# Kernel optimization log

Measured on AMD Instinct MI355X. Metric: run time of the kernel, lower is better.

Reference implementation:

```python
import jax, jax.numpy as jnp
import numpy as np

NUM_HEADS = 8


def _conv1(x, w, b):
    # 1x1x1 Conv3d == per-voxel channel linear map. x: [B,C,D,H,W], w: [O,C], b: [O]
    return jnp.einsum('bcdhw,oc->bodhw', x, w) + b[None, :, None, None, None]


def setup_inputs() -> dict:
    key = jax.random.key(0)
    ks = jax.random.split(key, 7)
    B, C, D, H, W = 1, 64, 16, 16, 16
    s = 0.02
    return {
        'decoder_features': jax.random.normal(ks[0], (B, C, D, H, W), jnp.float32),
        'mae_features': jax.random.normal(ks[1], (B, C, D, H, W), jnp.float32),
        'q_w': jax.random.normal(ks[2], (C, C), jnp.float32) * s,
        'q_b': jnp.zeros((C,), jnp.float32),
        'k_w': jax.random.normal(ks[3], (C, C), jnp.float32) * s,
        'k_b': jnp.zeros((C,), jnp.float32),
        'v_w': jax.random.normal(ks[4], (C, C), jnp.float32) * s,
        'v_b': jnp.zeros((C,), jnp.float32),
        'o_w': jax.random.normal(ks[5], (C, C), jnp.float32) * s,
        'o_b': jnp.zeros((C,), jnp.float32),
    }


def reference(decoder_features, mae_features, q_w, q_b, k_w, k_b, v_w, v_b, o_w, o_b):
    B, C, D, H, W = decoder_features.shape
    nh = NUM_HEADS
    hd = C // nh
    N = D * H * W
    scale = hd ** -0.5

    def split_heads(x):
        # [B,C,D,H,W] -> [B, nh, N, hd]
        return x.reshape(B, nh, hd, N).transpose(0, 1, 3, 2)

    Q = split_heads(_conv1(decoder_features, q_w, q_b))
    K = split_heads(_conv1(mae_features, k_w, k_b))
    V = split_heads(_conv1(mae_features, v_w, v_b))

    attn = jax.nn.softmax(jnp.einsum('bhnc,bhmc->bhnm', Q, K) * scale, axis=-1)
    out = jnp.einsum('bhnm,bhmc->bhnc', attn, V)  # [B, nh, N, hd]
    out = out.transpose(0, 1, 3, 2).reshape(B, C, D, H, W)
    return _conv1(out, o_w, o_b)
```

## Files before the change

kernel.cpp:

```cpp
#include <hip/hip_runtime.h>
#include <hip/hip_bf16.h>
#include <math.h>


#define N_VOX 4096
#define NH 8
#define QSCALE 0.51010813f

typedef unsigned short ushort_t;
typedef __attribute__((ext_vector_type(8))) short bf16x8;
typedef __attribute__((ext_vector_type(16))) float f32x16;

__device__ __forceinline__ unsigned short f2bf(float f) {
  union { float f; unsigned u; } v; v.f = f;
  unsigned r = v.u + 0x7FFFu + ((v.u >> 16) & 1u);
  return (unsigned short)(r >> 16);
}
__device__ __forceinline__ unsigned pk2bf(float a, float b) {
  __hip_bfloat162 h = __float22bfloat162_rn(float2{a, b});
  union { __hip_bfloat162 h; unsigned u; } c; c.h = h;
  return c.u;
}
__device__ __forceinline__ float ex2(float x) { return __builtin_amdgcn_exp2f(x); }

__global__ __launch_bounds__(256) void qkv_pack(
    const float* __restrict__ dec, const float* __restrict__ mae,
    const float* __restrict__ qw, const float* __restrict__ qb_,
    const float* __restrict__ kw, const float* __restrict__ kb,
    const float* __restrict__ vw, const float* __restrict__ vb,
    ushort_t* __restrict__ Qp, ushort_t* __restrict__ Kp,
    ushort_t* __restrict__ VtP, ushort_t* __restrict__ zeroblk) {
  const int bx = blockIdx.x;
  const int n = blockIdx.y * 256 + threadIdx.x;

  if (bx < 8) {
    const int h = bx;
    float x[64];
#pragma unroll
    for (int c = 0; c < 64; ++c) x[c] = dec[c * N_VOX + n];
    float qv[8];
#pragma unroll
    for (int j = 0; j < 8; ++j) {
      const int o = h * 8 + j;
      float a = qb_[o];
#pragma unroll
      for (int c = 0; c < 64; ++c) a = fmaf(x[c], qw[o * 64 + c], a);
      qv[j] = a * QSCALE;
    }
    uint4 pk;
    pk.x = pk2bf(qv[0], qv[1]); pk.y = pk2bf(qv[2], qv[3]);
    pk.z = pk2bf(qv[4], qv[5]); pk.w = pk2bf(qv[6], qv[7]);
    *(uint4*)(Qp + ((size_t)h * N_VOX + n) * 8) = pk;
  } else {
    const int h = bx - 8;
    float x[64];
#pragma unroll
    for (int c = 0; c < 64; ++c) x[c] = mae[c * N_VOX + n];
    float kv[8], vv[8];
#pragma unroll
    for (int j = 0; j < 8; ++j) {
      const int o = h * 8 + j;
      float a = kb[o], b = vb[o];
#pragma unroll
      for (int c = 0; c < 64; ++c) {
        a = fmaf(x[c], kw[o * 64 + c], a);
        b = fmaf(x[c], vw[o * 64 + c], b);
      }
      kv[j] = a; vv[j] = b;
    }
    uint4 pk;
    pk.x = pk2bf(kv[0], kv[1]); pk.y = pk2bf(kv[2], kv[3]);
    pk.z = pk2bf(kv[4], kv[5]); pk.w = pk2bf(kv[6], kv[7]);
    *(uint4*)(Kp + ((size_t)h * N_VOX + n) * 8) = pk;

    const size_t base =
        (((size_t)h * (N_VOX / 16) + (n >> 4)) * 64 + ((n >> 3) & 1) * 32) * 8 +
        (n & 7);
#pragma unroll
    for (int d = 0; d < 8; ++d) VtP[base + (size_t)d * 8] = f2bf(vv[d]);
    VtP[base + 8 * 8] = 0x3F80;
    if (h == 0 && n < 8) zeroblk[n] = 0;
  }
}

__global__ __launch_bounds__(256, 4) void attn_mfma(
    const ushort_t* __restrict__ Qp, const ushort_t* __restrict__ Kp,
    const ushort_t* __restrict__ VtP, const ushort_t* __restrict__ zeroblk,
    float* __restrict__ o_part, int kps) {
  const int tid = threadIdx.x;
  const int lane = tid & 63;
  const int wave = tid >> 6;
  const int l31 = lane & 31;
  const int lhalf = lane >> 5;
  const int h = blockIdx.y;
  const int ks = blockIdx.z;
  const int qb = blockIdx.x * 256 + wave * 64;

  __shared__ ushort_t P_lds[8][32 * 36];

  bf16x8 qfrag0 = *(const bf16x8*)(Qp + ((size_t)h * N_VOX + qb + l31) * 8);
  bf16x8 qfrag1 = *(const bf16x8*)(Qp + ((size_t)h * N_VOX + qb + 32 + l31) * 8);

  f32x16 zf, acc0, acc1;
#pragma unroll
  for (int i = 0; i < 16; ++i) { zf[i] = 0.f; acc0[i] = 0.f; acc1[i] = 0.f; }

  const ushort_t* KpH = Kp + (size_t)h * N_VOX * 8;
  const ushort_t* VtPH = VtP + (size_t)h * (N_VOX / 16) * 64 * 8;
  ushort_t* pb0 = &P_lds[wave * 2 + 0][l31 * 36];
  ushort_t* pb1 = &P_lds[wave * 2 + 1][l31 * 36];

  const int kbeg = ks * kps;
  const ushort_t* kzero = zeroblk;

  bf16x8 kf = *(const bf16x8*)(lhalf ? kzero
                                     : (KpH + (size_t)(kbeg + l31) * 8));
  bf16x8 vf0 = *(const bf16x8*)(VtPH + ((size_t)((kbeg >> 4) + 0) * 64 + lane) * 8);
  bf16x8 vf1 = *(const bf16x8*)(VtPH + ((size_t)((kbeg >> 4) + 1) * 64 + lane) * 8);

  for (int kk = 0; kk < kps; kk += 32) {
    const int knext = (kk + 32 < kps) ? (kbeg + kk + 32) : (kbeg + kk);
    bf16x8 kf_n = *(const bf16x8*)(lhalf ? kzero
                                         : (KpH + (size_t)(knext + l31) * 8));
    bf16x8 vf0_n = *(const bf16x8*)(VtPH + ((size_t)((knext >> 4) + 0) * 64 + lane) * 8);
    bf16x8 vf1_n = *(const bf16x8*)(VtPH + ((size_t)((knext >> 4) + 1) * 64 + lane) * 8);

    f32x16 s0 = __builtin_amdgcn_mfma_f32_32x32x16_bf16(kf, qfrag0, zf, 0, 0, 0);
    f32x16 s1 = __builtin_amdgcn_mfma_f32_32x32x16_bf16(kf, qfrag1, zf, 0, 0, 0);

#pragma unroll
    for (int G = 0; G < 4; ++G) {
      uint2 w;
      w.x = pk2bf(ex2(s0[G * 4 + 0]), ex2(s0[G * 4 + 1]));
      w.y = pk2bf(ex2(s0[G * 4 + 2]), ex2(s0[G * 4 + 3]));
      *(uint2*)(pb0 + G * 8 + lhalf * 4) = w;
    }
#pragma unroll
    for (int G = 0; G < 4; ++G) {
      uint2 w;
      w.x = pk2bf(ex2(s1[G * 4 + 0]), ex2(s1[G * 4 + 1]));
      w.y = pk2bf(ex2(s1[G * 4 + 2]), ex2(s1[G * 4 + 3]));
      *(uint2*)(pb1 + G * 8 + lhalf * 4) = w;
    }

#pragma unroll
    for (int grp = 0; grp < 2; ++grp) {
      union { bf16x8 v; uint2 u[2]; } p0, p1;
      p0.u[0] = *(const uint2*)(pb0 + grp * 16 + lhalf * 8);
      p0.u[1] = *(const uint2*)(pb0 + grp * 16 + lhalf * 8 + 4);
      p1.u[0] = *(const uint2*)(pb1 + grp * 16 + lhalf * 8);
      p1.u[1] = *(const uint2*)(pb1 + grp * 16 + lhalf * 8 + 4);
      const bf16x8 vf = grp ? vf1 : vf0;
      acc0 = __builtin_amdgcn_mfma_f32_32x32x16_bf16(p0.v, vf, acc0, 0, 0, 0);
      acc1 = __builtin_amdgcn_mfma_f32_32x32x16_bf16(p1.v, vf, acc1, 0, 0, 0);
    }

    kf = kf_n; vf0 = vf0_n; vf1 = vf1_n;
  }

  if (l31 < 9) {
    float* ob = o_part + ((size_t)(ks * NH + h) * 9 + l31) * N_VOX;
#pragma unroll
    for (int t = 0; t < 2; ++t) {
      const f32x16 a = t ? acc1 : acc0;
      const int qst = qb + t * 32 + 4 * lhalf;
#pragma unroll
      for (int G = 0; G < 4; ++G) {
        float4 v4 = make_float4(a[G * 4 + 0], a[G * 4 + 1], a[G * 4 + 2], a[G * 4 + 3]);
        *(float4*)(ob + qst + 8 * G) = v4;
      }
    }
  }
}

__global__ __launch_bounds__(256) void combine(
    const float* __restrict__ o_part, float* __restrict__ ocomb, int KS) {
  const int t = blockIdx.x * 256 + threadIdx.x;
  const int c = t >> 12, n = t & (N_VOX - 1);
  const int h = c >> 3, d = c & 7;
  float so = 0.f, sl = 0.f;
  for (int s = 0; s < KS; ++s) {
    const float* base = o_part + ((size_t)(s * NH + h) * 9) * N_VOX;
    so += base[d * N_VOX + n];
    sl += base[8 * N_VOX + n];
  }
  ocomb[(size_t)c * N_VOX + n] = so / sl;
}

__global__ __launch_bounds__(256) void out_proj(
    const float* __restrict__ ocomb, const float* __restrict__ ow,
    const float* __restrict__ obias, float* __restrict__ out) {
  const int og = blockIdx.x;
  const int n = blockIdx.y * 256 + threadIdx.x;
  float x[64];
#pragma unroll
  for (int c = 0; c < 64; ++c) x[c] = ocomb[c * N_VOX + n];
#pragma unroll
  for (int j = 0; j < 8; ++j) {
    const int o = og * 8 + j;
    float acc = obias[o];
#pragma unroll
    for (int c = 0; c < 64; ++c) acc = fmaf(x[c], ow[o * 64 + c], acc);
    out[o * N_VOX + n] = acc;
  }
}

extern "C" void kernel_launch(void* const* d_in, const int* in_sizes, int n_in,
                              void* d_out, int out_size, void* d_ws, size_t ws_size,
                              hipStream_t stream) {
  const float* dec = (const float*)d_in[0];
  const float* mae = (const float*)d_in[1];
  const float* qw = (const float*)d_in[2];
  const float* qb = (const float*)d_in[3];
  const float* kw = (const float*)d_in[4];
  const float* kb = (const float*)d_in[5];
  const float* vw = (const float*)d_in[6];
  const float* vb = (const float*)d_in[7];
  const float* ow = (const float*)d_in[8];
  const float* ob = (const float*)d_in[9];
  float* out = (float*)d_out;
  char* ws = (char*)d_ws;

  const size_t OFF_QP = 0;
  const size_t OFF_KP = 0x80000;
  const size_t OFF_ZERO = 0x100000;
  const size_t OFF_VT = 0x101000;
  const size_t OFF_OPART = 0x301000;

  int KS = 16;
  while (KS > 1) {
    size_t need = OFF_OPART + (size_t)KS * NH * 9 * N_VOX * 4 + 64ull * N_VOX * 4;
    if (need <= ws_size) break;
    KS >>= 1;
  }
  const size_t OFF_OCOMB = OFF_OPART + (size_t)KS * NH * 9 * N_VOX * 4;

  ushort_t* Qp = (ushort_t*)(ws + OFF_QP);
  ushort_t* Kp = (ushort_t*)(ws + OFF_KP);
  ushort_t* zb = (ushort_t*)(ws + OFF_ZERO);
  ushort_t* VtP = (ushort_t*)(ws + OFF_VT);
  float* o_part = (float*)(ws + OFF_OPART);
  float* ocomb = (float*)(ws + OFF_OCOMB);

  qkv_pack<<<dim3(16, 16), 256, 0, stream>>>(dec, mae, qw, qb, kw, kb, vw, vb,
                                             Qp, Kp, VtP, zb);
  attn_mfma<<<dim3(16, 8, KS), 256, 0, stream>>>(Qp, Kp, VtP, zb, o_part,
                                                 N_VOX / KS);
  combine<<<1024, 256, 0, stream>>>(o_part, ocomb, KS);
  out_proj<<<dim3(8, 16), 256, 0, stream>>>(ocomb, ow, ob, out);
}
```

Baseline: 137.0 us.

## Fuse combine into output projection, fix split count, zero-pad K rows

Merges the split-K combine and the output 1x1 projection into one kernel that sums partial outputs and normalises them on the fly, removing the intermediate buffer and one launch. The split count is fixed at compile time to 8 (previously up to 16, depending on workspace size). K rows are padded to 16 elements with zeros so the upper half-wave loads zeros directly instead of branching to a shared zero block. The software prefetch of K/V in the attention loop is dropped in favour of plain per-iteration loads. The fused kernel rereads o_part once for each of the 8 output groups, and the lost prefetch may expose load latency.

```diff
diff --git a/kernel.cpp b/kernel.cpp
--- a/kernel.cpp
+++ b/kernel.cpp
@@ -5,6 +5,8 @@
 
 #define N_VOX 4096
 #define NH 8
+#define KS 8
+#define KPS (N_VOX / KS)
 #define QSCALE 0.51010813f
 
 typedef unsigned short ushort_t;
@@ -28,8 +30,8 @@
     const float* __restrict__ qw, const float* __restrict__ qb_,
     const float* __restrict__ kw, const float* __restrict__ kb,
     const float* __restrict__ vw, const float* __restrict__ vb,
-    ushort_t* __restrict__ Qp, ushort_t* __restrict__ Kp,
-    ushort_t* __restrict__ VtP, ushort_t* __restrict__ zeroblk) {
+    ushort_t* __restrict__ Qp, ushort_t* __restrict__ KpZ,
+    ushort_t* __restrict__ VtP) {
   const int bx = blockIdx.x;
   const int n = blockIdx.y * 256 + threadIdx.x;
 
@@ -60,18 +62,20 @@
 #pragma unroll
     for (int j = 0; j < 8; ++j) {
       const int o = h * 8 + j;
-      float a = kb[o], b = vb[o];
+      float a = kb[o], v = vb[o];
 #pragma unroll
       for (int c = 0; c < 64; ++c) {
         a = fmaf(x[c], kw[o * 64 + c], a);
-        b = fmaf(x[c], vw[o * 64 + c], b);
+        v = fmaf(x[c], vw[o * 64 + c], v);
       }
-      kv[j] = a; vv[j] = b;
+      kv[j] = a; vv[j] = v;
     }
     uint4 pk;
     pk.x = pk2bf(kv[0], kv[1]); pk.y = pk2bf(kv[2], kv[3]);
     pk.z = pk2bf(kv[4], kv[5]); pk.w = pk2bf(kv[6], kv[7]);
-    *(uint4*)(Kp + ((size_t)h * N_VOX + n) * 8) = pk;
+    ushort_t* krow = KpZ + ((size_t)h * N_VOX + n) * 16;
+    *(uint4*)(krow) = pk;
+    *(uint4*)(krow + 8) = make_uint4(0, 0, 0, 0);
 
     const size_t base =
         (((size_t)h * (N_VOX / 16) + (n >> 4)) * 64 + ((n >> 3) & 1) * 32) * 8 +
@@ -79,14 +83,12 @@
 #pragma unroll
     for (int d = 0; d < 8; ++d) VtP[base + (size_t)d * 8] = f2bf(vv[d]);
     VtP[base + 8 * 8] = 0x3F80;
-    if (h == 0 && n < 8) zeroblk[n] = 0;
   }
 }
 
 __global__ __launch_bounds__(256, 4) void attn_mfma(
-    const ushort_t* __restrict__ Qp, const ushort_t* __restrict__ Kp,
-    const ushort_t* __restrict__ VtP, const ushort_t* __restrict__ zeroblk,
-    float* __restrict__ o_part, int kps) {
+    const ushort_t* __restrict__ Qp, const ushort_t* __restrict__ KpZ,
+    const ushort_t* __restrict__ VtP, float* __restrict__ o_part) {
   const int tid = threadIdx.x;
   const int lane = tid & 63;
   const int wave = tid >> 6;
@@ -105,25 +107,18 @@
 #pragma unroll
   for (int i = 0; i < 16; ++i) { zf[i] = 0.f; acc0[i] = 0.f; acc1[i] = 0.f; }
 
-  const ushort_t* KpH = Kp + (size_t)h * N_VOX * 8;
+  const ushort_t* KpH = KpZ + (size_t)h * N_VOX * 16 + lhalf * 8;
   const ushort_t* VtPH = VtP + (size_t)h * (N_VOX / 16) * 64 * 8;
   ushort_t* pb0 = &P_lds[wave * 2 + 0][l31 * 36];
   ushort_t* pb1 = &P_lds[wave * 2 + 1][l31 * 36];
-
-  const int kbeg = ks * kps;
-  const ushort_t* kzero = zeroblk;
-
-  bf16x8 kf = *(const bf16x8*)(lhalf ? kzero
-                                     : (KpH + (size_t)(kbeg + l31) * 8));
-  bf16x8 vf0 = *(const bf16x8*)(VtPH + ((size_t)((kbeg >> 4) + 0) * 64 + lane) * 8);
-  bf16x8 vf1 = *(const bf16x8*)(VtPH + ((size_t)((kbeg >> 4) + 1) * 64 + lane) * 8);
-
-  for (int kk = 0; kk < kps; kk += 32) {
-    const int knext = (kk + 32 < kps) ? (kbeg + kk + 32) : (kbeg + kk);
-    bf16x8 kf_n = *(const bf16x8*)(lhalf ? kzero
-                                         : (KpH + (size_t)(knext + l31) * 8));
-    bf16x8 vf0_n = *(const bf16x8*)(VtPH + ((size_t)((knext >> 4) + 0) * 64 + lane) * 8);
-    bf16x8 vf1_n = *(const bf16x8*)(VtPH + ((size_t)((knext >> 4) + 1) * 64 + lane) * 8);
+  const int kbeg = ks * KPS;
+
+#pragma unroll 1
+  for (int kk = 0; kk < KPS; kk += 32) {
+    const int kcur = kbeg + kk;
+    bf16x8 kf = *(const bf16x8*)(KpH + (size_t)(kcur + l31) * 16);
+    bf16x8 vf0 = *(const bf16x8*)(VtPH + ((size_t)((kcur >> 4) + 0) * 64 + lane) * 8);
+    bf16x8 vf1 = *(const bf16x8*)(VtPH + ((size_t)((kcur >> 4) + 1) * 64 + lane) * 8);
 
     f32x16 s0 = __builtin_amdgcn_mfma_f32_32x32x16_bf16(kf, qfrag0, zf, 0, 0, 0);
     f32x16 s1 = __builtin_amdgcn_mfma_f32_32x32x16_bf16(kf, qfrag1, zf, 0, 0, 0);
@@ -154,8 +149,6 @@
       acc0 = __builtin_amdgcn_mfma_f32_32x32x16_bf16(p0.v, vf, acc0, 0, 0, 0);
       acc1 = __builtin_amdgcn_mfma_f32_32x32x16_bf16(p1.v, vf, acc1, 0, 0, 0);
     }
-
-    kf = kf_n; vf0 = vf0_n; vf1 = vf1_n;
   }
 
   if (l31 < 9) {
@@ -173,36 +166,40 @@
   }
 }
 
-__global__ __launch_bounds__(256) void combine(
-    const float* __restrict__ o_part, float* __restrict__ ocomb, int KS) {
-  const int t = blockIdx.x * 256 + threadIdx.x;
-  const int c = t >> 12, n = t & (N_VOX - 1);
-  const int h = c >> 3, d = c & 7;
-  float so = 0.f, sl = 0.f;
-  for (int s = 0; s < KS; ++s) {
-    const float* base = o_part + ((size_t)(s * NH + h) * 9) * N_VOX;
-    so += base[d * N_VOX + n];
-    sl += base[8 * N_VOX + n];
-  }
-  ocomb[(size_t)c * N_VOX + n] = so / sl;
-}
-
-__global__ __launch_bounds__(256) void out_proj(
-    const float* __restrict__ ocomb, const float* __restrict__ ow,
+__global__ __launch_bounds__(256) void combine_proj(
+    const float* __restrict__ o_part, const float* __restrict__ ow,
     const float* __restrict__ obias, float* __restrict__ out) {
   const int og = blockIdx.x;
   const int n = blockIdx.y * 256 + threadIdx.x;
-  float x[64];
-#pragma unroll
-  for (int c = 0; c < 64; ++c) x[c] = ocomb[c * N_VOX + n];
-#pragma unroll
-  for (int j = 0; j < 8; ++j) {
-    const int o = og * 8 + j;
-    float acc = obias[o];
-#pragma unroll
-    for (int c = 0; c < 64; ++c) acc = fmaf(x[c], ow[o * 64 + c], acc);
-    out[o * N_VOX + n] = acc;
-  }
+
+  float rinv[NH];
+#pragma unroll
+  for (int h = 0; h < NH; ++h) {
+    float l = 0.f;
+#pragma unroll
+    for (int s = 0; s < KS; ++s)
+      l += o_part[((size_t)(s * NH + h) * 9 + 8) * N_VOX + n];
+    rinv[h] = 1.0f / l;
+  }
+
+  float acc[8];
+#pragma unroll
+  for (int j = 0; j < 8; ++j) acc[j] = obias[og * 8 + j];
+
+#pragma unroll 2
+  for (int c = 0; c < 64; ++c) {
+    const int h = c >> 3, d = c & 7;
+    float so = 0.f;
+#pragma unroll
+    for (int s = 0; s < KS; ++s)
+      so += o_part[((size_t)(s * NH + h) * 9 + d) * N_VOX + n];
+    const float x = so * rinv[h];
+#pragma unroll
+    for (int j = 0; j < 8; ++j)
+      acc[j] = fmaf(x, ow[(og * 8 + j) * 64 + c], acc[j]);
+  }
+#pragma unroll
+  for (int j = 0; j < 8; ++j) out[(size_t)(og * 8 + j) * N_VOX + n] = acc[j];
 }
 
 extern "C" void kernel_launch(void* const* d_in, const int* in_sizes, int n_in,
@@ -223,29 +220,16 @@
 
   const size_t OFF_QP = 0;
   const size_t OFF_KP = 0x80000;
-  const size_t OFF_ZERO = 0x100000;
-  const size_t OFF_VT = 0x101000;
-  const size_t OFF_OPART = 0x301000;
-
-  int KS = 16;
-  while (KS > 1) {
-    size_t need = OFF_OPART + (size_t)KS * NH * 9 * N_VOX * 4 + 64ull * N_VOX * 4;
-    if (need <= ws_size) break;
-    KS >>= 1;
-  }
-  const size_t OFF_OCOMB = OFF_OPART + (size_t)KS * NH * 9 * N_VOX * 4;
+  const size_t OFF_VT = 0x180000;
+  const size_t OFF_OPART = 0x380000;
 
   ushort_t* Qp = (ushort_t*)(ws + OFF_QP);
-  ushort_t* Kp = (ushort_t*)(ws + OFF_KP);
-  ushort_t* zb = (ushort_t*)(ws + OFF_ZERO);
+  ushort_t* KpZ = (ushort_t*)(ws + OFF_KP);
   ushort_t* VtP = (ushort_t*)(ws + OFF_VT);
   float* o_part = (float*)(ws + OFF_OPART);
-  float* ocomb = (float*)(ws + OFF_OCOMB);
 
   qkv_pack<<<dim3(16, 16), 256, 0, stream>>>(dec, mae, qw, qb, kw, kb, vw, vb,
-                                             Qp, Kp, VtP, zb);
-  attn_mfma<<<dim3(16, 8, KS), 256, 0, stream>>>(Qp, Kp, VtP, zb, o_part,
-                                                 N_VOX / KS);
-  combine<<<1024, 256, 0, stream>>>(o_part, ocomb, KS);
-  out_proj<<<dim3(8, 16), 256, 0, stream>>>(ocomb, ow, ob, out);
-}
+                                             Qp, KpZ, VtP);
+  attn_mfma<<<dim3(16, 8, KS), 256, 0, stream>>>(Qp, KpZ, VtP, o_part);
+  combine_proj<<<dim3(8, 16), 256, 0, stream>>>(o_part, ow, ob, out);
+}
```

Result: slower. 154.9 us (+13.1%).
